# Kernel tuning notes

Hardware: AMD Instinct MI355X
Metric: run time of the kernel (lower is better)

Reference implementation:

```python
import jax, jax.numpy as jnp
import numpy as np

N, E, F = 32768, 524288, 16          # nodes, edges, num_filters
S_IN, V_IN = 64, 32                  # input irreps: 64x0e + 32x1o  (dim 64 + 96 = 160)
NRBF = 32                            # radial basis size of f_ij
LN2 = float(np.log(2.0))

def ssp(x):
    # shifted softplus, the standard SchNet activation
    return jax.nn.softplus(x) - LN2

def setup_inputs() -> dict:
    key = jax.random.key(0)
    ks = jax.random.split(key, 16)
    x = jax.random.normal(ks[0], (N, S_IN + 3 * V_IN), jnp.float32)
    idx_i = jax.random.randint(ks[1], (E,), 0, N)
    idx_j = jax.random.randint(ks[2], (E,), 0, N)
    f_ij = jax.random.normal(ks[3], (E, NRBF), jnp.float32)
    rcut_ij = jax.random.uniform(ks[4], (E,), jnp.float32)
    Yr_ij = jax.random.normal(ks[5], (E, 4), jnp.float32)  # 1x0e + 1x1o
    # equivariant Linear 1: (64x0e+32x1o) -> num_filters*(1x0e+1x1o) = 16x0e+16x1o
    W1_0e = jax.random.normal(ks[6], (S_IN, F), jnp.float32)
    W1_1o = jax.random.normal(ks[7], (V_IN, F), jnp.float32)
    # filter MLP: NRBF -> F -> num_irreps(6*F)
    mW1 = jax.random.normal(ks[8], (NRBF, F), jnp.float32) / np.sqrt(NRBF)
    mb1 = jnp.zeros((F,), jnp.float32)
    mW2 = jax.random.normal(ks[9], (F, 6 * F), jnp.float32) / np.sqrt(F)
    mb2 = jnp.zeros((6 * F,), jnp.float32)
    # equivariant Linear 2: (2Fx0e+2Fx1o+Fx1e+Fx2e) -> input irreps (1e/2e paths drop)
    W2_0e = jax.random.normal(ks[10], (2 * F, S_IN), jnp.float32)
    W2_1o = jax.random.normal(ks[11], (2 * F, V_IN), jnp.float32)
    # equivariant Linear 3: input irreps -> input irreps
    W3_0e = jax.random.normal(ks[12], (S_IN, S_IN), jnp.float32)
    W3_1o = jax.random.normal(ks[13], (V_IN, V_IN), jnp.float32)
    return dict(x=x, f_ij=f_ij, rcut_ij=rcut_ij, Yr_ij=Yr_ij,
                W1_0e=W1_0e, W1_1o=W1_1o, mW1=mW1, mb1=mb1, mW2=mW2, mb2=mb2,
                W2_0e=W2_0e, W2_1o=W2_1o, W3_0e=W3_0e, W3_1o=W3_1o,
                idx_i=idx_i, idx_j=idx_j)

def reference(x, f_ij, rcut_ij, Yr_ij, W1_0e, W1_1o, mW1, mb1, mW2, mb2,
              W2_0e, W2_1o, W3_0e, W3_1o, idx_i, idx_j):
    n = x.shape[0]
    s = x[:, :S_IN]                                  # [N, 64]  0e channels
    v = x[:, S_IN:].reshape(n, V_IN, 3)              # [N, 32, 3] 1o channels
    # Linear 1 (per-irrep channel mixing, e3nn fan-in normalization)
    s1 = (s @ W1_0e) / np.sqrt(S_IN)                 # [N, F]
    v1 = jnp.einsum('ncd,cf->nfd', v, W1_1o) / np.sqrt(V_IN)  # [N, F, 3]
    # gather neighbor features (x_j = x[idx_j], mul_to_axis -> per-filter irreps)
    sj = s1[idx_j]                                   # [E, F]
    vj = v1[idx_j]                                   # [E, F, 3]
    y0 = Yr_ij[:, 0]                                 # [E]
    y1 = Yr_ij[:, 1:4]                               # [E, 3]
    # tensor product (0e+1o) x (0e+1o) -> 2x0e + 2x1o + 1x1e + 1x2e, per filter
    o0a = sj * y0[:, None]                                            # 0e: 0e x 0e
    o0b = jnp.einsum('efd,ed->ef', vj, y1) / np.sqrt(3.0)             # 0e: 1o.1o
    o1a = sj[:, :, None] * y1[:, None, :]                             # 1o: 0e x 1o
    o1b = vj * y0[:, None, None]                                      # 1o: 1o x 0e
    o1e = jnp.cross(vj, y1[:, None, :]) / np.sqrt(2.0)                # 1e: 1o ^ 1o
    ux, uy, uz = vj[..., 0], vj[..., 1], vj[..., 2]
    wx, wy, wz = y1[:, None, 0], y1[:, None, 1], y1[:, None, 2]
    o2 = jnp.stack([(ux * wy + uy * wx) / np.sqrt(2.0),
                    (uy * wz + uz * wy) / np.sqrt(2.0),
                    (2.0 * uz * wz - ux * wx - uy * wy) / np.sqrt(6.0),
                    (ux * wz + uz * wx) / np.sqrt(2.0),
                    (ux * wx - uy * wy) / np.sqrt(2.0)], axis=-1)      # 2e [E, F, 5]
    # filter MLP on radial features, gated by cutoff; one scalar per irrep
    W = ssp(f_ij @ mW1 + mb1) @ mW2 + mb2            # [E, 6F]
    W = W * rcut_ij[:, None]
    w0a, w0b, w1a, w1b, w1e, w2 = (W[:, k * F:(k + 1) * F] for k in range(6))
    seg = lambda z: jax.ops.segment_sum(z, idx_i, num_segments=N)
    # modulate + scatter-sum into center atoms
    n0a = seg(o0a * w0a); n0b = seg(o0b * w0b)                          # [N, F]
    n1a = seg(o1a * w1a[:, :, None]); n1b = seg(o1b * w1b[:, :, None])  # [N, F, 3]
    n1e = seg(o1e * w1e[:, :, None])                                    # [N, F, 3] (dropped by Linear 2)
    n2 = seg(o2 * w2[:, :, None])                                       # [N, F, 5] (dropped by Linear 2)
    n0 = jnp.concatenate([n0a, n0b], axis=-1)        # [N, 2F] 0e
    n1 = jnp.concatenate([n1a, n1b], axis=1)         # [N, 2F, 3] 1o
    del n1e, n2  # no matching output irrep in input_irreps -> e3nn Linear drops them
    # Linear 2 back to input irreps
    s2 = (n0 @ W2_0e) / np.sqrt(2 * F)               # [N, 64]
    v2 = jnp.einsum('nfd,fc->ncd', n1, W2_1o) / np.sqrt(2 * F)  # [N, 32, 3]
    # scalar activation on l=0 only
    s2 = ssp(s2)
    # Linear 3
    s3 = (s2 @ W3_0e) / np.sqrt(S_IN)
    v3 = jnp.einsum('ncd,ce->ned', v2, W3_1o) / np.sqrt(V_IN)
    return jnp.concatenate([s3, v3.reshape(n, -1)], axis=-1)  # [N, 160]
```

## Files before the change

kernel.cpp:

```cpp
#include <hip/hip_runtime.h>
#include <math.h>

#define NN 32768
#define NE 524288

__device__ __forceinline__ float sspf(float x) {
    float r = fmaxf(x, 0.0f) + log1pf(expf(-fabsf(x)));
    return r - 0.69314718055994530942f;
}

__global__ __launch_bounds__(256) void hist_kernel(
    const int* __restrict__ idx_i, int* __restrict__ counts)
{
    int e = blockIdx.x * 256 + threadIdx.x;
    atomicAdd(&counts[idx_i[e]], 1);
}

__global__ __launch_bounds__(1024) void scan_kernel(
    const int* __restrict__ counts, int* __restrict__ start, int* __restrict__ cursor)
{
    __shared__ int tmp[1024];
    int tid = threadIdx.x;
    int base = tid * 32;
    int local[32];
    int sum = 0;
    const int4* c4 = (const int4*)(counts + base);
#pragma unroll
    for (int q = 0; q < 8; q++) {
        int4 v = c4[q];
        local[q*4+0] = sum; sum += v.x;
        local[q*4+1] = sum; sum += v.y;
        local[q*4+2] = sum; sum += v.z;
        local[q*4+3] = sum; sum += v.w;
    }
    tmp[tid] = sum;
    __syncthreads();
    for (int off = 1; off < 1024; off <<= 1) {
        int v = 0;
        if (tid >= off) v = tmp[tid - off];
        __syncthreads();
        if (tid >= off) tmp[tid] += v;
        __syncthreads();
    }
    int excl = tmp[tid] - sum;
#pragma unroll
    for (int k = 0; k < 32; k++) {
        int s = excl + local[k];
        start[base + k] = s;
        cursor[base + k] = s;
    }
    if (tid == 1023) start[NN] = tmp[1023];
}

__global__ __launch_bounds__(256) void pack_kernel(
    const float* __restrict__ f_ij,
    const float* __restrict__ rcut_ij,
    const float* __restrict__ Yr,
    const int*   __restrict__ idx_i,
    const int*   __restrict__ idx_j,
    const float* __restrict__ mW1,
    const float* __restrict__ mb1,
    int* __restrict__ cursor,
    float* __restrict__ epack)
{
    __shared__ float sW1[512];
    __shared__ float sb1[16];
    int t = threadIdx.x;
    for (int k = t; k < 512; k += 256) sW1[k] = mW1[k];
    if (t < 16) sb1[t] = mb1[t];
    __syncthreads();

    int e = blockIdx.x * 256 + t;
    float h[16];
#pragma unroll
    for (int f = 0; f < 16; f++) h[f] = sb1[f];
    const float4* frow = (const float4*)(f_ij + (size_t)e * 32);
#pragma unroll
    for (int rq = 0; rq < 8; rq++) {
        float4 fv = frow[rq];
        int r = rq * 4;
#pragma unroll
        for (int f = 0; f < 16; f++)
            h[f] += fv.x * sW1[(r+0)*16+f] + fv.y * sW1[(r+1)*16+f]
                  + fv.z * sW1[(r+2)*16+f] + fv.w * sW1[(r+3)*16+f];
    }
    float rc = rcut_ij[e];
#pragma unroll
    for (int f = 0; f < 16; f++) h[f] = sspf(h[f]) * rc;

    int i = idx_i[e];
    int j = idx_j[e];
    float4 y = ((const float4*)Yr)[e];
    int slot = atomicAdd(&cursor[i], 1);

    float* rec = epack + (size_t)slot * 24;
    float4* r4 = (float4*)rec;
#pragma unroll
    for (int q = 0; q < 4; q++) r4[q] = ((float4*)h)[q];
    r4[4] = y;
    rec[20] = rc;
    rec[21] = __int_as_float(j);
    rec[22] = 0.f;
    rec[23] = 0.f;
}

__global__ __launch_bounds__(256) void embed_kernel(
    const float* __restrict__ x,
    const float* __restrict__ W1s,
    const float* __restrict__ W1v,
    float* __restrict__ embed)
{
    __shared__ float sWs[1024];
    __shared__ float sWv[512];
    int t = threadIdx.x;
    for (int k = t; k < 1024; k += 256) sWs[k] = W1s[k];
    for (int k = t; k < 512;  k += 256) sWv[k] = W1v[k];
    __syncthreads();

    int n = blockIdx.x * 256 + t;
    const float* xr = x + (size_t)n * 160;

    float s1[16];
#pragma unroll
    for (int f = 0; f < 16; f++) s1[f] = 0.f;
#pragma unroll
    for (int cq = 0; cq < 16; cq++) {
        float4 sv = ((const float4*)xr)[cq];
        int c = cq * 4;
#pragma unroll
        for (int f = 0; f < 16; f++) {
            s1[f] += sv.x * sWs[(c+0)*16+f] + sv.y * sWs[(c+1)*16+f]
                   + sv.z * sWs[(c+2)*16+f] + sv.w * sWs[(c+3)*16+f];
        }
    }

    float v1[48];
#pragma unroll
    for (int k = 0; k < 48; k++) v1[k] = 0.f;
#pragma unroll
    for (int q = 0; q < 24; q++) {
        float4 vv = ((const float4*)(xr + 64))[q];
        float vals[4] = {vv.x, vv.y, vv.z, vv.w};
#pragma unroll
        for (int u = 0; u < 4; u++) {
            int m = q * 4 + u;
            int c = m / 3, d = m % 3;
            float val = vals[u];
#pragma unroll
            for (int f = 0; f < 16; f++)
                v1[f*3+d] += val * sWv[c*16+f];
        }
    }

    float ob[64];
#pragma unroll
    for (int f = 0; f < 16; f++) ob[f] = s1[f] * 0.125f;
    const float is32 = 0.17677669529663688f;
#pragma unroll
    for (int k = 0; k < 48; k++) ob[16+k] = v1[k] * is32;

    float4* eo = (float4*)(embed + (size_t)n * 64);
#pragma unroll
    for (int q = 0; q < 16; q++) eo[q] = ((float4*)ob)[q];
}

__global__ __launch_bounds__(256) void nodeagg_kernel(
    const float* __restrict__ embed,
    const float* __restrict__ epack,
    const int*   __restrict__ start,
    const float* __restrict__ mW2,
    const float* __restrict__ mb2,
    float* __restrict__ acc)
{
    __shared__ float sW2[1024];
    int t = threadIdx.x;
    for (int k = t; k < 1024; k += 256)
        sW2[k] = mW2[(k >> 6) * 96 + (k & 63)];
    __syncthreads();

    int gid = blockIdx.x * 256 + t;
    int node = gid >> 4;
    int f = gid & 15;

    float wga[16], wgb[16], wgc[16], wgd[16];
#pragma unroll
    for (int k = 0; k < 16; k++) {
        wga[k] = sW2[k*64 + f];
        wgb[k] = sW2[k*64 + 16 + f];
        wgc[k] = sW2[k*64 + 32 + f];
        wgd[k] = sW2[k*64 + 48 + f];
    }
    float b0a = mb2[f], b0b = mb2[16+f], b1a = mb2[32+f], b1b = mb2[48+f];

    float aa = 0.f, ab = 0.f;
    float A1a0 = 0.f, A1a1 = 0.f, A1a2 = 0.f;
    float A1b0 = 0.f, A1b1 = 0.f, A1b2 = 0.f;

    int s0 = start[node];
    int s1 = start[node+1];

    for (int q = s0; q < s1; q++) {
        const float* rec = epack + (size_t)q * 24;
        const float4* r4 = (const float4*)rec;
        float4 h0 = r4[0], h1 = r4[1], h2 = r4[2], h3 = r4[3];
        float4 y  = r4[4];
        float rc  = rec[20];
        int j = __float_as_int(rec[21]);

        const float* em = embed + (size_t)j * 64;
        float sj = em[f];
        float vx = em[16 + f*3 + 0];
        float vy = em[16 + f*3 + 1];
        float vz = em[16 + f*3 + 2];

        float w0a = rc*b0a, w0b = rc*b0b, w1a = rc*b1a, w1b = rc*b1b;
        float h[16] = {h0.x,h0.y,h0.z,h0.w, h1.x,h1.y,h1.z,h1.w,
                       h2.x,h2.y,h2.z,h2.w, h3.x,h3.y,h3.z,h3.w};
#pragma unroll
        for (int k = 0; k < 16; k++) {
            w0a += h[k] * wga[k];
            w0b += h[k] * wgb[k];
            w1a += h[k] * wgc[k];
            w1b += h[k] * wgd[k];
        }

        aa += sj * y.x * w0a;
        ab += (vx*y.y + vy*y.z + vz*y.w) * w0b;
        float sw = sj * w1a;
        A1a0 += sw * y.y;
        A1a1 += sw * y.z;
        A1a2 += sw * y.w;
        float yw = y.x * w1b;
        A1b0 += vx * yw;
        A1b1 += vy * yw;
        A1b2 += vz * yw;
    }

    const float is3 = 0.5773502691896258f;
    float* o = acc + (size_t)node * 128;
    o[f] = aa;
    o[16 + f] = ab * is3;
    o[32 + f*3 + 0] = A1a0;
    o[32 + f*3 + 1] = A1a1;
    o[32 + f*3 + 2] = A1a2;
    o[80 + f*3 + 0] = A1b0;
    o[80 + f*3 + 1] = A1b1;
    o[80 + f*3 + 2] = A1b2;
}

__global__ __launch_bounds__(256) void out_kernel(
    const float* __restrict__ acc,
    const float* __restrict__ W2s,
    const float* __restrict__ W2v,
    const float* __restrict__ W3s,
    const float* __restrict__ W3v,
    float* __restrict__ out)
{
    __shared__ float lds[4][288];
    int t = threadIdx.x;
    int wv = t >> 6, ln = t & 63;
    int n = blockIdx.x * 4 + wv;
    float* L = lds[wv];
    const float* a = acc + (size_t)n * 128;
    L[ln] = a[ln];
    L[64+ln] = a[64+ln];
    __syncthreads();

    const float is32 = 0.17677669529663688f;

    float s_acc = 0.f;
#pragma unroll
    for (int g = 0; g < 32; g++) s_acc += L[g] * W2s[g*64 + ln];
    float s2 = sspf(s_acc * is32);

    float v2a = 0.f, v2b = 0.f;
    int c1 = ln / 3, d1 = ln % 3;
    int o2i = ln + 64;
    int c2 = o2i / 3, d2 = o2i % 3;
#pragma unroll
    for (int fq = 0; fq < 32; fq++) {
        v2a += L[32 + fq*3 + d1] * W2v[fq*32 + c1];
        if (ln < 32) v2b += L[32 + fq*3 + d2] * W2v[fq*32 + c2];
    }

    L[128 + ln] = s2;
    L[192 + ln] = v2a * is32;
    if (ln < 32) L[192 + 64 + ln] = v2b * is32;
    __syncthreads();

    float s3 = 0.f;
#pragma unroll
    for (int k = 0; k < 64; k++) s3 += L[128+k] * W3s[k*64 + ln];
    out[(size_t)n*160 + ln] = s3 * 0.125f;

    float a1 = 0.f;
#pragma unroll
    for (int c = 0; c < 32; c++) a1 += L[192 + c*3 + d1] * W3v[c*32 + c1];
    out[(size_t)n*160 + 64 + ln] = a1 * is32;
    if (ln < 32) {
        float a2 = 0.f;
#pragma unroll
        for (int c = 0; c < 32; c++) a2 += L[192 + c*3 + d2] * W3v[c*32 + c2];
        out[(size_t)n*160 + 64 + o2i] = a2 * is32;
    }
}

extern "C" void kernel_launch(void* const* d_in, const int* in_sizes, int n_in,
                              void* d_out, int out_size, void* d_ws, size_t ws_size,
                              hipStream_t stream) {
    const float* x     = (const float*)d_in[0];
    const float* f_ij  = (const float*)d_in[1];
    const float* rcut  = (const float*)d_in[2];
    const float* Yr    = (const float*)d_in[3];
    const float* W1s   = (const float*)d_in[4];
    const float* W1v   = (const float*)d_in[5];
    const float* mW1   = (const float*)d_in[6];
    const float* mb1   = (const float*)d_in[7];
    const float* mW2   = (const float*)d_in[8];
    const float* mb2   = (const float*)d_in[9];
    const float* W2s   = (const float*)d_in[10];
    const float* W2v   = (const float*)d_in[11];
    const float* W3s   = (const float*)d_in[12];
    const float* W3v   = (const float*)d_in[13];
    const int*   idx_i = (const int*)d_in[14];
    const int*   idx_j = (const int*)d_in[15];
    float* out = (float*)d_out;

    float* fws   = (float*)d_ws;
    float* embed = fws;
    float* acc   = embed + (size_t)NN * 64;
    float* epack = acc   + (size_t)NN * 128;
    int* ibase   = (int*)(epack + (size_t)NE * 24);
    int* counts  = ibase;
    int* start   = counts + NN;
    int* cursor  = start + NN + 1;

    hipMemsetAsync(counts, 0, (size_t)NN * sizeof(int), stream);
    hist_kernel<<<NE/256, 256, 0, stream>>>(idx_i, counts);
    scan_kernel<<<1, 1024, 0, stream>>>(counts, start, cursor);
    pack_kernel<<<NE/256, 256, 0, stream>>>(f_ij, rcut, Yr, idx_i, idx_j,
                                            mW1, mb1, cursor, epack);
    embed_kernel<<<NN/256, 256, 0, stream>>>(x, W1s, W1v, embed);
    nodeagg_kernel<<<(NN*16)/256, 256, 0, stream>>>(embed, epack, start, mW2, mb2, acc);
    out_kernel<<<NN/4, 256, 0, stream>>>(acc, W2s, W2v, W3s, W3v, out);
}
```

Measured before the change: 394.4 us.

## Transpose vector layout to component-major and stage output weights in LDS

The embed and acc buffers now store 1o channels component-major (x/y/z planes of 16), so the gather in nodeagg reads contiguous addresses across the 16 filter lanes and the acc writes coalesce. The out kernel now handles 64 nodes per block over 512 blocks, loading all W2/W3 weights into shared memory once per block instead of reading them from global memory for every node. This adds about 33KB of LDS per block and an extra barrier per iteration, and it reduces the number of blocks in flight.

After: 375.5 us. -4.8%, faster.

```diff
diff --git a/kernel.cpp b/kernel.cpp
--- a/kernel.cpp
+++ b/kernel.cpp
@@ -153,11 +153,14 @@
     }
 
     float ob[64];
-#pragma unroll
-    for (int f = 0; f < 16; f++) ob[f] = s1[f] * 0.125f;
     const float is32 = 0.17677669529663688f;
 #pragma unroll
-    for (int k = 0; k < 48; k++) ob[16+k] = v1[k] * is32;
+    for (int f = 0; f < 16; f++) {
+        ob[f]      = s1[f] * 0.125f;
+        ob[16 + f] = v1[f*3+0] * is32;
+        ob[32 + f] = v1[f*3+1] * is32;
+        ob[48 + f] = v1[f*3+2] * is32;
+    }
 
     float4* eo = (float4*)(embed + (size_t)n * 64);
 #pragma unroll
@@ -209,9 +212,9 @@
 
         const float* em = embed + (size_t)j * 64;
         float sj = em[f];
-        float vx = em[16 + f*3 + 0];
-        float vy = em[16 + f*3 + 1];
-        float vz = em[16 + f*3 + 2];
+        float vx = em[16 + f];
+        float vy = em[32 + f];
+        float vz = em[48 + f];
 
         float w0a = rc*b0a, w0b = rc*b0b, w1a = rc*b1a, w1b = rc*b1b;
         float h[16] = {h0.x,h0.y,h0.z,h0.w, h1.x,h1.y,h1.z,h1.w,
@@ -238,14 +241,14 @@
 
     const float is3 = 0.5773502691896258f;
     float* o = acc + (size_t)node * 128;
-    o[f] = aa;
-    o[16 + f] = ab * is3;
-    o[32 + f*3 + 0] = A1a0;
-    o[32 + f*3 + 1] = A1a1;
-    o[32 + f*3 + 2] = A1a2;
-    o[80 + f*3 + 0] = A1b0;
-    o[80 + f*3 + 1] = A1b1;
-    o[80 + f*3 + 2] = A1b2;
+    o[f]       = aa;
+    o[16 + f]  = ab * is3;
+    o[32 + f]  = A1a0;
+    o[48 + f]  = A1a1;
+    o[64 + f]  = A1a2;
+    o[80 + f]  = A1b0;
+    o[96 + f]  = A1b1;
+    o[112 + f] = A1b2;
 }
 
 __global__ __launch_bounds__(256) void out_kernel(
@@ -256,52 +259,72 @@
     const float* __restrict__ W3v,
     float* __restrict__ out)
 {
-    __shared__ float lds[4][288];
+    __shared__ float sW2s[2048];
+    __shared__ float sW2v[1024];
+    __shared__ float sW3s[4096];
+    __shared__ float sW3v[1024];
+    __shared__ float Lbuf[4][288];
     int t = threadIdx.x;
+    for (int k = t; k < 2048; k += 256) sW2s[k] = W2s[k];
+    for (int k = t; k < 1024; k += 256) sW2v[k] = W2v[k];
+    for (int k = t; k < 4096; k += 256) sW3s[k] = W3s[k];
+    for (int k = t; k < 1024; k += 256) sW3v[k] = W3v[k];
+    __syncthreads();
+
     int wv = t >> 6, ln = t & 63;
-    int n = blockIdx.x * 4 + wv;
-    float* L = lds[wv];
-    const float* a = acc + (size_t)n * 128;
-    L[ln] = a[ln];
-    L[64+ln] = a[64+ln];
-    __syncthreads();
-
+    float* L = Lbuf[wv];
     const float is32 = 0.17677669529663688f;
 
-    float s_acc = 0.f;
-#pragma unroll
-    for (int g = 0; g < 32; g++) s_acc += L[g] * W2s[g*64 + ln];
-    float s2 = sspf(s_acc * is32);
-
-    float v2a = 0.f, v2b = 0.f;
     int c1 = ln / 3, d1 = ln % 3;
-    int o2i = ln + 64;
+    int o2i = 64 + ln;
     int c2 = o2i / 3, d2 = o2i % 3;
-#pragma unroll
-    for (int fq = 0; fq < 32; fq++) {
-        v2a += L[32 + fq*3 + d1] * W2v[fq*32 + c1];
-        if (ln < 32) v2b += L[32 + fq*3 + d2] * W2v[fq*32 + c2];
-    }
-
-    L[128 + ln] = s2;
-    L[192 + ln] = v2a * is32;
-    if (ln < 32) L[192 + 64 + ln] = v2b * is32;
-    __syncthreads();
-
-    float s3 = 0.f;
-#pragma unroll
-    for (int k = 0; k < 64; k++) s3 += L[128+k] * W3s[k*64 + ln];
-    out[(size_t)n*160 + ln] = s3 * 0.125f;
-
-    float a1 = 0.f;
-#pragma unroll
-    for (int c = 0; c < 32; c++) a1 += L[192 + c*3 + d1] * W3v[c*32 + c1];
-    out[(size_t)n*160 + 64 + ln] = a1 * is32;
-    if (ln < 32) {
-        float a2 = 0.f;
-#pragma unroll
-        for (int c = 0; c < 32; c++) a2 += L[192 + c*3 + d2] * W3v[c*32 + c2];
-        out[(size_t)n*160 + 64 + o2i] = a2 * is32;
+
+    for (int it = 0; it < 16; it++) {
+        int n = blockIdx.x * 64 + it * 4 + wv;
+        const float* a = acc + (size_t)n * 128;
+        float2 av = ((const float2*)a)[ln];
+        ((float2*)L)[ln] = av;
+        __syncthreads();
+
+        float s_acc = 0.f;
+#pragma unroll
+        for (int g = 0; g < 32; g++) s_acc += L[g] * sW2s[g*64 + ln];
+        float s2 = sspf(s_acc * is32);
+
+        float v2a = 0.f, v2b = 0.f;
+        int ba1 = 32 + d1*16, bb1 = 80 + d1*16;
+        int ba2 = 32 + d2*16, bb2 = 80 + d2*16;
+#pragma unroll
+        for (int f = 0; f < 16; f++) {
+            v2a += L[ba1+f] * sW2v[f*32 + c1];
+            v2a += L[bb1+f] * sW2v[(16+f)*32 + c1];
+            if (ln < 32) {
+                v2b += L[ba2+f] * sW2v[f*32 + c2];
+                v2b += L[bb2+f] * sW2v[(16+f)*32 + c2];
+            }
+        }
+
+        L[128 + ln] = s2;
+        L[192 + ln] = v2a * is32;
+        if (ln < 32) L[192 + 64 + ln] = v2b * is32;
+        __syncthreads();
+
+        float s3 = 0.f;
+#pragma unroll
+        for (int k = 0; k < 64; k++) s3 += L[128+k] * sW3s[k*64 + ln];
+        out[(size_t)n*160 + ln] = s3 * 0.125f;
+
+        float a1 = 0.f;
+#pragma unroll
+        for (int c = 0; c < 32; c++) a1 += L[192 + c*3 + d1] * sW3v[c*32 + c1];
+        out[(size_t)n*160 + 64 + ln] = a1 * is32;
+        if (ln < 32) {
+            float a2 = 0.f;
+#pragma unroll
+            for (int c = 0; c < 32; c++) a2 += L[192 + c*3 + d2] * sW3v[c*32 + c2];
+            out[(size_t)n*160 + 64 + o2i] = a2 * is32;
+        }
+        __syncthreads();
     }
 }
 
@@ -342,5 +365,5 @@
                                             mW1, mb1, cursor, epack);
     embed_kernel<<<NN/256, 256, 0, stream>>>(x, W1s, W1v, embed);
     nodeagg_kernel<<<(NN*16)/256, 256, 0, stream>>>(embed, epack, start, mW2, mb2, acc);
-    out_kernel<<<NN/4, 256, 0, stream>>>(acc, W2s, W2v, W3s, W3v, out);
-}
+    out_kernel<<<512, 256, 0, stream>>>(acc, W2s, W2v, W3s, W3v, out);
+}
```
